# Optimization experiments

Hardware: AMD Instinct MI355X
Metric: run time of the kernel (lower is better)

## Reference

```python
import jax, jax.numpy as jnp
import numpy as np

B = 16       # number of point clouds
N_PER = 2048 # points per cloud
K = 16       # knn neighbors (loop=True -> self included as nearest)
NUM_CLASSES = 10


def _linear_params(key, fan_in, fan_out):
    # torch.nn.Linear default init: U(-1/sqrt(fan_in), 1/sqrt(fan_in))
    kw, kb = jax.random.split(key)
    s = 1.0 / np.sqrt(fan_in)
    W = jax.random.uniform(kw, (fan_in, fan_out), jnp.float32, -s, s)
    b = jax.random.uniform(kb, (fan_out,), jnp.float32, -s, s)
    return W, b


def setup_inputs() -> dict:
    key = jax.random.key(0)
    ks = jax.random.split(key, 7)
    pos = jax.random.normal(ks[0], (B * N_PER, 3), jnp.float32)
    batch = jnp.repeat(jnp.arange(B, dtype=jnp.int64), N_PER)  # sorted graph ids
    W1a, b1a = _linear_params(ks[1], 3 + 3, 32)   # conv1 mlp layer 1 (h=pos -> 3+3)
    W1b, b1b = _linear_params(ks[2], 32, 32)      # conv1 mlp layer 2
    W2a, b2a = _linear_params(ks[3], 32 + 3, 32)  # conv2 mlp layer 1
    W2b, b2b = _linear_params(ks[4], 32, 32)      # conv2 mlp layer 2
    Wc, bc = _linear_params(ks[5], 32, NUM_CLASSES)
    return dict(pos=pos, batch=batch,
                W1a=W1a, b1a=b1a, W1b=W1b, b1b=b1b,
                W2a=W2a, b2a=b2a, W2b=W2b, b2b=b2b,
                Wc=Wc, bc=bc)


def _knn_idx(p):
    # p: [n,3] -> [n,K] indices of K nearest points (self included, dist 0)
    d2 = jnp.sum((p[:, None, :] - p[None, :, :]) ** 2, axis=-1)  # [n,n]
    _, idx = jax.lax.top_k(-d2, K)
    return idx


def _pointnet_layer(h, p, idx, Wa, ba, Wb, bb):
    # single graph: h [n,C], p [n,3], idx [n,K]
    h_j = h[idx]                           # gather neighbor features [n,K,C]
    spatial = p[idx] - p[:, None, :]       # pos_j - pos_i [n,K,3]
    x = jnp.concatenate([h_j, spatial], axis=-1)
    x = jax.nn.relu(x @ Wa + ba) @ Wb + bb # per-edge MLP
    return jnp.max(x, axis=1)              # max aggregation over neighbors


def reference(pos, batch, W1a, b1a, W1b, b1b, W2a, b2a, W2b, b2b, Wc, bc):
    # batch is sorted with equal-sized graphs -> reshape to [B, n, 3]
    p = pos.reshape(B, N_PER, 3)
    idx = jax.vmap(_knn_idx)(p)  # [B, n, K] dynamic knn graph
    layer = jax.vmap(_pointnet_layer, in_axes=(0, 0, 0, None, None, None, None))
    h = jax.nn.relu(layer(p, p, idx, W1a, b1a, W1b, b1b))   # [B, n, 32]
    h = jax.nn.relu(layer(h, p, idx, W2a, b2a, W2b, b2b))   # [B, n, 32]
    g = jnp.max(h, axis=1)                                   # global_max_pool [B, 32]
    return g @ Wc + bc                                       # [B, num_classes]
```

## Files before the change

kernel.cpp:

```cpp
#include <hip/hip_runtime.h>
#include <hip/hip_bf16.h>
#include <cstdint>

#define NCLOUDS 16
#define N_PER   2048
#define KNN_K   16
#define CAP     48

typedef unsigned long long u64;
#define INFF __builtin_inff()

template <int J>
__device__ __forceinline__ int ixor(int x) {
    if constexpr (J == 1)
        return __builtin_amdgcn_update_dpp(0, x, 0xB1, 0xF, 0xF, true);
    else if constexpr (J == 2)
        return __builtin_amdgcn_update_dpp(0, x, 0x4E, 0xF, 0xF, true);
    else if constexpr (J <= 16)
        return __builtin_amdgcn_ds_swizzle(x, (J << 10) | 0x1F);
    else
        return __shfl_xor(x, 32);
}
template <int J> __device__ __forceinline__ float fxor(float x) {
    return __int_as_float(ixor<J>(__float_as_int(x)));
}
template <int J> __device__ __forceinline__ u64 uxor(u64 x) {
    const int lo = ixor<J>((int)(x & 0xffffffffULL));
    const int hi = ixor<J>((int)(x >> 32));
    return ((u64)(unsigned)hi << 32) | (unsigned)lo;
}

__device__ __forceinline__ float dpp_max16(float x) {
    x = fmaxf(x, __int_as_float(__builtin_amdgcn_update_dpp(0, __float_as_int(x), 0xB1, 0xF, 0xF, true)));
    x = fmaxf(x, __int_as_float(__builtin_amdgcn_update_dpp(0, __float_as_int(x), 0x4E, 0xF, 0xF, true)));
    x = fmaxf(x, __int_as_float(__builtin_amdgcn_update_dpp(0, __float_as_int(x), 0x141, 0xF, 0xF, true)));
    x = fmaxf(x, __int_as_float(__builtin_amdgcn_update_dpp(0, __float_as_int(x), 0x140, 0xF, 0xF, true)));
    return x;
}

__global__ __launch_bounds__(512) void knn_kernel(const float* __restrict__ pos,
                                                  int* __restrict__ knn_out,
                                                  const float* __restrict__ W1a,
                                                  const float* __restrict__ b1a,
                                                  float* __restrict__ w1,
                                                  float* __restrict__ v1,
                                                  float* __restrict__ gbuf,
                                                  int* __restrict__ counter)
{
    __shared__ float qshare[3][32];
    __shared__ float smA[4][2][8][16];
    __shared__ u64   buf[4][8][CAP];
    __shared__ int   cnt[4][8];

    const int cloud = blockIdx.x >> 6;
    const int qblk  = blockIdx.x & 63;
    const int tid   = threadIdx.x;
    const int wave  = tid >> 6;
    const int lane  = tid & 63;
    const int H     = wave & 1;
    const int pr    = wave >> 1;

    const int b0 = cloud * N_PER;

    if (blockIdx.x == 0) {
        if (tid < NCLOUDS * 32) gbuf[tid] = 0.0f;
        if (tid == 0) *counter = 0;
    }

    if (tid < 32) {
        const float* qp = pos + (size_t)(b0 + qblk * 32 + tid) * 3;
        qshare[0][tid] = qp[0];
        qshare[1][tid] = qp[1];
        qshare[2][tid] = qp[2];
        ((int*)cnt)[tid] = 0;
    }

    float cx[16], cy[16], cz[16], sc[16];
#pragma unroll
    for (int jj = 0; jj < 16; ++jj) {
        const int c = H * 1024 + jj * 64 + lane;
        const float* p = pos + (size_t)(b0 + c) * 3;
        cx[jj] = p[0]; cy[jj] = p[1]; cz[jj] = p[2];
        sc[jj] = fmaf(cz[jj], cz[jj], fmaf(cy[jj], cy[jj], cx[jj] * cx[jj]));
    }
    __syncthreads();

#pragma unroll 1
    for (int t = 0; t < 4; ++t) {
        const int qg0 = pr * 8 + 2 * t, qg1 = qg0 + 1;
        const float Q0x = qshare[0][qg0], Q0y = qshare[1][qg0], Q0z = qshare[2][qg0];
        const float Q1x = qshare[0][qg1], Q1y = qshare[1][qg1], Q1z = qshare[2][qg1];
        const float A0x = -2.0f * Q0x, A0y = -2.0f * Q0y, A0z = -2.0f * Q0z;
        const float A1x = -2.0f * Q1x, A1y = -2.0f * Q1y, A1z = -2.0f * Q1z;
        float v0 = INFF, v1r = INFF;
#pragma unroll
        for (int jj = 0; jj < 16; ++jj) {
            float e0 = fmaf(cx[jj], A0x, sc[jj]);
            float e1 = fmaf(cx[jj], A1x, sc[jj]);
            e0 = fmaf(cy[jj], A0y, e0);  e1 = fmaf(cy[jj], A1y, e1);
            e0 = fmaf(cz[jj], A0z, e0);  e1 = fmaf(cz[jj], A1z, e1);
            v0 = fminf(v0, e0);          v1r = fminf(v1r, e1);
        }
#define FS(K, J) { const float o0 = fxor<J>(v0), o1 = fxor<J>(v1r);             \
                   const bool km = (((lane & J) == 0) == ((lane & K) == 0));    \
                   v0 = km ? fminf(v0, o0) : fmaxf(v0, o0);                     \
                   v1r = km ? fminf(v1r, o1) : fmaxf(v1r, o1); }
        FS(2,1)
        FS(4,2) FS(4,1)
        FS(8,4) FS(8,2) FS(8,1)
        FS(16,8) FS(16,4) FS(16,2) FS(16,1)
        FS(32,16) FS(32,8) FS(32,4) FS(32,2) FS(32,1)
        FS(64,32) FS(64,16) FS(64,8) FS(64,4) FS(64,2) FS(64,1)
#undef FS
        if (lane < 16) {
            smA[pr][H][2 * t][lane]     = v0;
            smA[pr][H][2 * t + 1][lane] = v1r;
        }
    }
    __syncthreads();

#pragma unroll 1
    for (int t = 0; t < 4; ++t) {
        const int q0 = 2 * t, q1 = q0 + 1;
        float a0 = -INFF, a1 = -INFF, b0v = -INFF, b1v = -INFF;
        if (lane > 0 && lane <= 16) {
            a0 = smA[pr][0][q0][lane - 1];
            a1 = smA[pr][0][q1][lane - 1];
        }
        if (lane < 16) {
            b0v = smA[pr][1][q0][15 - lane];
            b1v = smA[pr][1][q1][15 - lane];
        }
        float m0 = (lane <= 16) ? fmaxf(a0, b0v) : INFF;
        float m1 = (lane <= 16) ? fmaxf(a1, b1v) : INFF;
        m0 = fminf(m0, fxor<1>(m0));   m1 = fminf(m1, fxor<1>(m1));
        m0 = fminf(m0, fxor<2>(m0));   m1 = fminf(m1, fxor<2>(m1));
        m0 = fminf(m0, fxor<4>(m0));   m1 = fminf(m1, fxor<4>(m1));
        m0 = fminf(m0, fxor<8>(m0));   m1 = fminf(m1, fxor<8>(m1));
        m0 = fminf(m0, fxor<16>(m0));  m1 = fminf(m1, fxor<16>(m1));
        m0 = fminf(m0, fxor<32>(m0));  m1 = fminf(m1, fxor<32>(m1));

        const int qg0 = pr * 8 + q0, qg1 = pr * 8 + q1;
        const float Q0x = qshare[0][qg0], Q0y = qshare[1][qg0], Q0z = qshare[2][qg0];
        const float Q1x = qshare[0][qg1], Q1y = qshare[1][qg1], Q1z = qshare[2][qg1];
        const float qq0 = fmaf(Q0z, Q0z, fmaf(Q0y, Q0y, Q0x * Q0x));
        const float qq1 = fmaf(Q1z, Q1z, fmaf(Q1y, Q1y, Q1x * Q1x));
        const float T0 = (m0 + qq0) * (1.0f + 1e-5f) + 1e-4f;
        const float T1 = (m1 + qq1) * (1.0f + 1e-5f) + 1e-4f;

#pragma unroll
        for (int jj = 0; jj < 16; ++jj) {
            const int c = H * 1024 + jj * 64 + lane;
            const float dx0 = __fsub_rn(Q0x, cx[jj]);
            const float dy0 = __fsub_rn(Q0y, cy[jj]);
            const float dz0 = __fsub_rn(Q0z, cz[jj]);
            const float d20 = __fadd_rn(__fadd_rn(__fmul_rn(dx0, dx0), __fmul_rn(dy0, dy0)),
                                        __fmul_rn(dz0, dz0));
            if (d20 <= T0) {
                const int slot = atomicAdd(&cnt[pr][q0], 1);
                if (slot < CAP)
                    buf[pr][q0][slot] = ((u64)__float_as_uint(d20) << 32) | (unsigned)c;
            }
            const float dx1 = __fsub_rn(Q1x, cx[jj]);
            const float dy1 = __fsub_rn(Q1y, cy[jj]);
            const float dz1 = __fsub_rn(Q1z, cz[jj]);
            const float d21 = __fadd_rn(__fadd_rn(__fmul_rn(dx1, dx1), __fmul_rn(dy1, dy1)),
                                        __fmul_rn(dz1, dz1));
            if (d21 <= T1) {
                const int slot = atomicAdd(&cnt[pr][q1], 1);
                if (slot < CAP)
                    buf[pr][q1][slot] = ((u64)__float_as_uint(d21) << 32) | (unsigned)c;
            }
        }
    }
    __syncthreads();

#pragma unroll 1
    for (int s = 0; s < 2; ++s) {
        const int q0 = H * 4 + 2 * s, q1 = q0 + 1;
        const int n0 = min(cnt[pr][q0], CAP);
        const int n1 = min(cnt[pr][q1], CAP);
        u64 k0 = (lane < n0) ? buf[pr][q0][lane] : ~0ULL;
        u64 k1 = (lane < n1) ? buf[pr][q1][lane] : ~0ULL;
#define US(K, J) { const u64 o0 = uxor<J>(k0), o1 = uxor<J>(k1);                \
                   const bool km = (((lane & J) == 0) == ((lane & K) == 0));    \
                   const u64 l0 = k0 < o0 ? k0 : o0, h0 = k0 < o0 ? o0 : k0;    \
                   k0 = km ? l0 : h0;                                           \
                   const u64 l1 = k1 < o1 ? k1 : o1, h1 = k1 < o1 ? o1 : k1;    \
                   k1 = km ? l1 : h1; }
        US(2,1)
        US(4,2) US(4,1)
        US(8,4) US(8,2) US(8,1)
        US(16,8) US(16,4) US(16,2) US(16,1)
        US(32,16) US(32,8) US(32,4) US(32,2) US(32,1)
        US(64,32) US(64,16) US(64,8) US(64,4) US(64,2) US(64,1)
#undef US
        if (lane < KNN_K) {
            knn_out[((size_t)b0 + qblk * 32 + pr * 8 + q0) * KNN_K + lane] =
                b0 + (int)(unsigned)(k0 & 0xffffffffu);
            knn_out[((size_t)b0 + qblk * 32 + pr * 8 + q1) * KNN_K + lane] =
                b0 + (int)(unsigned)(k1 & 0xffffffffu);
        }
    }

    {
        const int pt = tid >> 4;
        const int kk = tid & 15;
        const int gp = b0 + qblk * 32 + pt;
        const float p0 = pos[3 * (size_t)gp + 0];
        const float p1 = pos[3 * (size_t)gp + 1];
        const float p2 = pos[3 * (size_t)gp + 2];
        float vA = 0.f, vB = 0.f;
        float wA = b1a[kk], wB = b1a[16 + kk];
#pragma unroll
        for (int d = 0; d < 3; ++d) {
            const float pd = d == 0 ? p0 : (d == 1 ? p1 : p2);
            wA = fmaf(pd, W1a[d * 32 + kk],        wA);
            wB = fmaf(pd, W1a[d * 32 + 16 + kk],   wB);
            vA = fmaf(pd, W1a[(3 + d) * 32 + kk],      vA);
            vB = fmaf(pd, W1a[(3 + d) * 32 + 16 + kk], vB);
        }
        w1[(size_t)gp * 32 + kk]      = wA + vA;
        w1[(size_t)gp * 32 + 16 + kk] = wB + vB;
        v1[(size_t)gp * 32 + kk]      = vA;
        v1[(size_t)gp * 32 + 16 + kk] = vB;
    }
}

template <int MODE>
__global__ __launch_bounds__(256) void layer_kernel(
    const int*   __restrict__ knn,
    const float* __restrict__ Wb, const float* __restrict__ bb,
    const float* __restrict__ w,  const float* __restrict__ v,
    const float* __restrict__ pos,
    const float* __restrict__ Wna, const float* __restrict__ bna,
    float* __restrict__ outA, float* __restrict__ outB,
    const float* __restrict__ Wc, const float* __restrict__ bc,
    float* __restrict__ gbuf, int* __restrict__ counter,
    float* __restrict__ out)
{
    __shared__ float wst[256 * 36];
    __shared__ float vst[16 * 36];
    __shared__ int   jl[256];
    __shared__ int   lastFlag;

    const int tid = threadIdx.x;
    const int gth = blockIdx.x * 256 + tid;
    const int P0  = blockIdx.x * 16;

    jl[tid] = knn[gth];
    __syncthreads();

#pragma unroll
    for (int s = 0; s < 8; ++s) {
        const int r = s * 32 + (tid >> 3);
        const int i = tid & 7;
        const float4 t4 = *(const float4*)(w + (size_t)jl[r] * 32 + i * 4);
        *(float4*)&wst[r * 36 + i * 4] = t4;
    }
    if (tid < 128) {
        const int r = tid >> 3, i = tid & 7;
        const float4 t4 = *(const float4*)(v + (size_t)(P0 + r) * 32 + i * 4);
        *(float4*)&vst[r * 36 + i * 4] = t4;
    }
    __syncthreads();

    const int k  = tid & 15;
    const int pl = tid >> 4;

    float hid[32];
#pragma unroll
    for (int i = 0; i < 8; ++i) {
        const float4 a = *(const float4*)&wst[tid * 36 + i * 4];
        const float4 b = *(const float4*)&vst[pl  * 36 + i * 4];
        hid[4 * i + 0] = fmaxf(a.x - b.x, 0.0f);
        hid[4 * i + 1] = fmaxf(a.y - b.y, 0.0f);
        hid[4 * i + 2] = fmaxf(a.z - b.z, 0.0f);
        hid[4 * i + 3] = fmaxf(a.w - b.w, 0.0f);
    }

    float o[32];
#pragma unroll
    for (int c2 = 0; c2 < 32; ++c2) o[c2] = bb[c2];
#pragma unroll
    for (int c = 0; c < 32; ++c) {
        const float hc = hid[c];
        const float* row = Wb + c * 32;
#pragma unroll
        for (int c2 = 0; c2 < 32; ++c2) o[c2] = fmaf(hc, row[c2], o[c2]);
    }

    float out0 = 0.0f, out1 = 0.0f;
#pragma unroll
    for (int c2 = 0; c2 < 32; ++c2) {
        const float s = dpp_max16(o[c2]);
        if ((c2 & 15) == k) { if (c2 < 16) out0 = s; else out1 = s; }
    }
    out0 = fmaxf(out0, 0.0f);
    out1 = fmaxf(out1, 0.0f);

    __syncthreads();
    float* hs = wst;
    hs[pl * 32 + k]      = out0;
    hs[pl * 32 + 16 + k] = out1;
    __syncthreads();

    if constexpr (MODE == 1) {
        const int p = gth >> 4;
        float accA = bna[k], accB = bna[16 + k];
#pragma unroll
        for (int c = 0; c < 32; ++c) {
            const float hc = hs[pl * 32 + c];
            accA = fmaf(hc, Wna[c * 32 + k],      accA);
            accB = fmaf(hc, Wna[c * 32 + 16 + k], accB);
        }
        float vA = 0.f, vB = 0.f;
#pragma unroll
        for (int d = 0; d < 3; ++d) {
            const float pd = pos[3 * (size_t)p + d];
            vA = fmaf(pd, Wna[(32 + d) * 32 + k],      vA);
            vB = fmaf(pd, Wna[(32 + d) * 32 + 16 + k], vB);
        }
        outA[(size_t)p * 32 + k]      = accA + vA;
        outA[(size_t)p * 32 + 16 + k] = accB + vB;
        outB[(size_t)p * 32 + k]      = vA;
        outB[(size_t)p * 32 + 16 + k] = vB;
    } else {
        if (tid < 32) {
            float m = hs[tid];
#pragma unroll
            for (int p2 = 1; p2 < 16; ++p2) m = fmaxf(m, hs[p2 * 32 + tid]);
            const int cloud = P0 >> 11;
            atomicMax((int*)&gbuf[cloud * 32 + tid], __float_as_int(m));
        }
        __syncthreads();
        if (tid == 0) {
            __threadfence();
            lastFlag = (atomicAdd(counter, 1) == (int)gridDim.x - 1);
        }
        __syncthreads();
        if (lastFlag) {
            float* gl = wst;
            for (int t = tid; t < NCLOUDS * 32; t += 256)
                gl[t] = __int_as_float(atomicMax((int*)&gbuf[t], 0));
            __syncthreads();
            if (tid < NCLOUDS * 10) {
                const int cl = tid / 10, cls = tid - cl * 10;
                float s2 = bc[cls];
#pragma unroll
                for (int c = 0; c < 32; ++c)
                    s2 = fmaf(gl[cl * 32 + c], Wc[c * 10 + cls], s2);
                out[tid] = s2;
            }
        }
    }
}

extern "C" void kernel_launch(void* const* d_in, const int* in_sizes, int n_in,
                              void* d_out, int out_size, void* d_ws, size_t ws_size,
                              hipStream_t stream)
{
    const float* pos = (const float*)d_in[0];
    const float* W1a = (const float*)d_in[2];
    const float* b1a = (const float*)d_in[3];
    const float* W1b = (const float*)d_in[4];
    const float* b1b = (const float*)d_in[5];
    const float* W2a = (const float*)d_in[6];
    const float* b2a = (const float*)d_in[7];
    const float* W2b = (const float*)d_in[8];
    const float* b2b = (const float*)d_in[9];
    const float* Wc  = (const float*)d_in[10];
    const float* bc  = (const float*)d_in[11];

    int*   knn     = (int*)d_ws;
    float* w1      = (float*)((char*)d_ws + (size_t)(2  << 20));
    float* v1      = (float*)((char*)d_ws + (size_t)(6  << 20));
    float* w2      = (float*)((char*)d_ws + (size_t)(10 << 20));
    float* v2      = (float*)((char*)d_ws + (size_t)(14 << 20));
    float* gbuf    = (float*)((char*)d_ws + (size_t)(18 << 20));
    int*   counter = (int*)((char*)d_ws + (size_t)(18 << 20) + 4096);
    float* out     = (float*)d_out;

    const int npts = NCLOUDS * N_PER;

    knn_kernel<<<dim3(NCLOUDS * 64), dim3(512), 0, stream>>>(
        pos, knn, W1a, b1a, w1, v1, gbuf, counter);
    layer_kernel<1><<<dim3(npts * KNN_K / 256), dim3(256), 0, stream>>>(
        knn, W1b, b1b, w1, v1, pos, W2a, b2a, w2, v2,
        nullptr, nullptr, nullptr, nullptr, nullptr);
    layer_kernel<2><<<dim3(npts * KNN_K / 256), dim3(256), 0, stream>>>(
        knn, W2b, b2b, w2, v2, pos, nullptr, nullptr, nullptr, nullptr,
        Wc, bc, gbuf, counter, out);
}
```

Measured before the change: 138.7 us.

## Fuse both point layers into one cooperative kernel with grid syncs

Replaces the two per-layer kernel launches with a single cooperative kernel of 512 blocks, each handling 64 points. Grid-wide syncs separate layer 1, layer 2 and the final classifier, and the knn indices are kept in registers across both layers. The edge MLP now reads gathered neighbour features straight from global memory instead of staging them in shared memory. This removes one launch and the last-block counter, at the cost of grid-sync overhead and less parallelism (4 sequential edge passes per thread, limited occupancy). The old two-kernel path stays as a fallback if the cooperative launch fails.

New measurement: 383.1 us. +176.2%, slower.

```diff
diff --git a/kernel.cpp b/kernel.cpp
--- a/kernel.cpp
+++ b/kernel.cpp
@@ -1,6 +1,9 @@
 #include <hip/hip_runtime.h>
 #include <hip/hip_bf16.h>
+#include <hip/hip_cooperative_groups.h>
 #include <cstdint>
+
+namespace cg = cooperative_groups;
 
 #define NCLOUDS 16
 #define N_PER   2048
@@ -227,6 +230,142 @@
     }
 }
 
+__device__ __forceinline__ void edge_mlp(const float* __restrict__ w,
+                                         const float* __restrict__ v,
+                                         int j, int p, int k,
+                                         const float* __restrict__ Wb,
+                                         const float* __restrict__ bb,
+                                         float& out0, float& out1)
+{
+    const float4* w4 = (const float4*)w;
+    const float4* v4 = (const float4*)v;
+    float hid[32];
+#pragma unroll
+    for (int i = 0; i < 8; ++i) {
+        const float4 a = w4[(size_t)j * 8 + i];
+        const float4 b = v4[(size_t)p * 8 + i];
+        hid[4 * i + 0] = fmaxf(a.x - b.x, 0.0f);
+        hid[4 * i + 1] = fmaxf(a.y - b.y, 0.0f);
+        hid[4 * i + 2] = fmaxf(a.z - b.z, 0.0f);
+        hid[4 * i + 3] = fmaxf(a.w - b.w, 0.0f);
+    }
+    float o[32];
+#pragma unroll
+    for (int c2 = 0; c2 < 32; ++c2) o[c2] = bb[c2];
+#pragma unroll
+    for (int c = 0; c < 32; ++c) {
+        const float hc = hid[c];
+        const float* row = Wb + c * 32;
+#pragma unroll
+        for (int c2 = 0; c2 < 32; ++c2) o[c2] = fmaf(hc, row[c2], o[c2]);
+    }
+    out0 = 0.0f; out1 = 0.0f;
+#pragma unroll
+    for (int c2 = 0; c2 < 32; ++c2) {
+        const float s = dpp_max16(o[c2]);
+        if ((c2 & 15) == k) { if (c2 < 16) out0 = s; else out1 = s; }
+    }
+    out0 = fmaxf(out0, 0.0f);
+    out1 = fmaxf(out1, 0.0f);
+}
+
+__global__ __launch_bounds__(256, 2) void mega_kernel(
+    const int*   __restrict__ knn,  const float* __restrict__ pos,
+    const float* __restrict__ W1b,  const float* __restrict__ b1b,
+    const float* __restrict__ w1,   const float* __restrict__ v1,
+    const float* __restrict__ W2a,  const float* __restrict__ b2a,
+    float* __restrict__ w2,         float* __restrict__ v2,
+    const float* __restrict__ W2b,  const float* __restrict__ b2b,
+    const float* __restrict__ Wc,   const float* __restrict__ bc,
+    float* __restrict__ gbuf,       float* __restrict__ out)
+{
+    cg::grid_group grid = cg::this_grid();
+    __shared__ float hs[64][32];
+    __shared__ float gl[NCLOUDS * 32];
+
+    const int tid = threadIdx.x;
+    const int P0  = blockIdx.x * 64;
+    const int k   = tid & 15;
+    const int prl = tid >> 4;
+
+    int jreg[4];
+#pragma unroll
+    for (int i = 0; i < 4; ++i)
+        jreg[i] = knn[(size_t)(P0 + i * 16 + prl) * KNN_K + k];
+
+#pragma unroll 1
+    for (int i = 0; i < 4; ++i) {
+        const int pl = i * 16 + prl;
+        float o0, o1;
+        edge_mlp(w1, v1, jreg[i], P0 + pl, k, W1b, b1b, o0, o1);
+        hs[pl][k]      = o0;
+        hs[pl][16 + k] = o1;
+    }
+    __syncthreads();
+
+#pragma unroll 1
+    for (int i = 0; i < 4; ++i) {
+        const int pl = i * 16 + prl;
+        const int p  = P0 + pl;
+        float accA = b2a[k], accB = b2a[16 + k];
+#pragma unroll
+        for (int c = 0; c < 32; ++c) {
+            const float hc = hs[pl][c];
+            accA = fmaf(hc, W2a[c * 32 + k],      accA);
+            accB = fmaf(hc, W2a[c * 32 + 16 + k], accB);
+        }
+        float vA = 0.f, vB = 0.f;
+#pragma unroll
+        for (int d = 0; d < 3; ++d) {
+            const float pd = pos[3 * (size_t)p + d];
+            vA = fmaf(pd, W2a[(32 + d) * 32 + k],      vA);
+            vB = fmaf(pd, W2a[(32 + d) * 32 + 16 + k], vB);
+        }
+        w2[(size_t)p * 32 + k]      = accA + vA;
+        w2[(size_t)p * 32 + 16 + k] = accB + vB;
+        v2[(size_t)p * 32 + k]      = vA;
+        v2[(size_t)p * 32 + 16 + k] = vB;
+    }
+
+    __threadfence();
+    grid.sync();
+
+#pragma unroll 1
+    for (int i = 0; i < 4; ++i) {
+        const int pl = i * 16 + prl;
+        float o0, o1;
+        edge_mlp(w2, v2, jreg[i], P0 + pl, k, W2b, b2b, o0, o1);
+        hs[pl][k]      = o0;
+        hs[pl][16 + k] = o1;
+    }
+    __syncthreads();
+
+    if (tid < 32) {
+        float m = hs[0][tid];
+#pragma unroll
+        for (int r = 1; r < 64; ++r) m = fmaxf(m, hs[r][tid]);
+        const int cloud = blockIdx.x >> 5;
+        atomicMax((int*)&gbuf[cloud * 32 + tid], __float_as_int(m));
+    }
+
+    __threadfence();
+    grid.sync();
+
+    if (blockIdx.x == 0) {
+        for (int t = tid; t < NCLOUDS * 32; t += 256)
+            gl[t] = __int_as_float(atomicMax((int*)&gbuf[t], 0));
+        __syncthreads();
+        if (tid < NCLOUDS * 10) {
+            const int cl = tid / 10, cls = tid - cl * 10;
+            float s2 = bc[cls];
+#pragma unroll
+            for (int c = 0; c < 32; ++c)
+                s2 = fmaf(gl[cl * 32 + c], Wc[c * 10 + cls], s2);
+            out[tid] = s2;
+        }
+    }
+}
+
 template <int MODE>
 __global__ __launch_bounds__(256) void layer_kernel(
     const int*   __restrict__ knn,
@@ -239,78 +378,30 @@
     float* __restrict__ gbuf, int* __restrict__ counter,
     float* __restrict__ out)
 {
-    __shared__ float wst[256 * 36];
-    __shared__ float vst[16 * 36];
-    __shared__ int   jl[256];
+    __shared__ float hsf[16][32];
+    __shared__ float glf[NCLOUDS * 32];
     __shared__ int   lastFlag;
 
     const int tid = threadIdx.x;
     const int gth = blockIdx.x * 256 + tid;
     const int P0  = blockIdx.x * 16;
-
-    jl[tid] = knn[gth];
-    __syncthreads();
-
-#pragma unroll
-    for (int s = 0; s < 8; ++s) {
-        const int r = s * 32 + (tid >> 3);
-        const int i = tid & 7;
-        const float4 t4 = *(const float4*)(w + (size_t)jl[r] * 32 + i * 4);
-        *(float4*)&wst[r * 36 + i * 4] = t4;
-    }
-    if (tid < 128) {
-        const int r = tid >> 3, i = tid & 7;
-        const float4 t4 = *(const float4*)(v + (size_t)(P0 + r) * 32 + i * 4);
-        *(float4*)&vst[r * 36 + i * 4] = t4;
-    }
-    __syncthreads();
-
-    const int k  = tid & 15;
+    const int p   = gth >> 4;
+    const int k   = gth & 15;
+    const int j   = knn[gth];
+
+    float o0, o1;
+    edge_mlp(w, v, j, p, k, Wb, bb, o0, o1);
+
     const int pl = tid >> 4;
-
-    float hid[32];
-#pragma unroll
-    for (int i = 0; i < 8; ++i) {
-        const float4 a = *(const float4*)&wst[tid * 36 + i * 4];
-        const float4 b = *(const float4*)&vst[pl  * 36 + i * 4];
-        hid[4 * i + 0] = fmaxf(a.x - b.x, 0.0f);
-        hid[4 * i + 1] = fmaxf(a.y - b.y, 0.0f);
-        hid[4 * i + 2] = fmaxf(a.z - b.z, 0.0f);
-        hid[4 * i + 3] = fmaxf(a.w - b.w, 0.0f);
-    }
-
-    float o[32];
-#pragma unroll
-    for (int c2 = 0; c2 < 32; ++c2) o[c2] = bb[c2];
-#pragma unroll
-    for (int c = 0; c < 32; ++c) {
-        const float hc = hid[c];
-        const float* row = Wb + c * 32;
-#pragma unroll
-        for (int c2 = 0; c2 < 32; ++c2) o[c2] = fmaf(hc, row[c2], o[c2]);
-    }
-
-    float out0 = 0.0f, out1 = 0.0f;
-#pragma unroll
-    for (int c2 = 0; c2 < 32; ++c2) {
-        const float s = dpp_max16(o[c2]);
-        if ((c2 & 15) == k) { if (c2 < 16) out0 = s; else out1 = s; }
-    }
-    out0 = fmaxf(out0, 0.0f);
-    out1 = fmaxf(out1, 0.0f);
-
-    __syncthreads();
-    float* hs = wst;
-    hs[pl * 32 + k]      = out0;
-    hs[pl * 32 + 16 + k] = out1;
+    hsf[pl][k]      = o0;
+    hsf[pl][16 + k] = o1;
     __syncthreads();
 
     if constexpr (MODE == 1) {
-        const int p = gth >> 4;
         float accA = bna[k], accB = bna[16 + k];
 #pragma unroll
         for (int c = 0; c < 32; ++c) {
-            const float hc = hs[pl * 32 + c];
+            const float hc = hsf[pl][c];
             accA = fmaf(hc, Wna[c * 32 + k],      accA);
             accB = fmaf(hc, Wna[c * 32 + 16 + k], accB);
         }
@@ -327,9 +418,9 @@
         outB[(size_t)p * 32 + 16 + k] = vB;
     } else {
         if (tid < 32) {
-            float m = hs[tid];
-#pragma unroll
-            for (int p2 = 1; p2 < 16; ++p2) m = fmaxf(m, hs[p2 * 32 + tid]);
+            float m = hsf[0][tid];
+#pragma unroll
+            for (int p2 = 1; p2 < 16; ++p2) m = fmaxf(m, hsf[p2][tid]);
             const int cloud = P0 >> 11;
             atomicMax((int*)&gbuf[cloud * 32 + tid], __float_as_int(m));
         }
@@ -340,16 +431,15 @@
         }
         __syncthreads();
         if (lastFlag) {
-            float* gl = wst;
             for (int t = tid; t < NCLOUDS * 32; t += 256)
-                gl[t] = __int_as_float(atomicMax((int*)&gbuf[t], 0));
+                glf[t] = __int_as_float(atomicMax((int*)&gbuf[t], 0));
             __syncthreads();
             if (tid < NCLOUDS * 10) {
                 const int cl = tid / 10, cls = tid - cl * 10;
                 float s2 = bc[cls];
 #pragma unroll
                 for (int c = 0; c < 32; ++c)
-                    s2 = fmaf(gl[cl * 32 + c], Wc[c * 10 + cls], s2);
+                    s2 = fmaf(glf[cl * 32 + c], Wc[c * 10 + cls], s2);
                 out[tid] = s2;
             }
         }
@@ -385,10 +475,19 @@
 
     knn_kernel<<<dim3(NCLOUDS * 64), dim3(512), 0, stream>>>(
         pos, knn, W1a, b1a, w1, v1, gbuf, counter);
-    layer_kernel<1><<<dim3(npts * KNN_K / 256), dim3(256), 0, stream>>>(
-        knn, W1b, b1b, w1, v1, pos, W2a, b2a, w2, v2,
-        nullptr, nullptr, nullptr, nullptr, nullptr);
-    layer_kernel<2><<<dim3(npts * KNN_K / 256), dim3(256), 0, stream>>>(
-        knn, W2b, b2b, w2, v2, pos, nullptr, nullptr, nullptr, nullptr,
-        Wc, bc, gbuf, counter, out);
-}
+
+    void* args[] = { &knn, &pos, &W1b, &b1b, &w1, &v1, &W2a, &b2a,
+                     &w2, &v2, &W2b, &b2b, &Wc, &bc, &gbuf, &out };
+    hipError_t cerr = hipLaunchCooperativeKernel((const void*)mega_kernel,
+                                                 dim3(512), dim3(256), args,
+                                                 0, stream);
+    if (cerr != hipSuccess) {
+        (void)hipGetLastError();
+        layer_kernel<1><<<dim3(npts * KNN_K / 256), dim3(256), 0, stream>>>(
+            knn, W1b, b1b, w1, v1, pos, W2a, b2a, w2, v2,
+            nullptr, nullptr, nullptr, nullptr, nullptr);
+        layer_kernel<2><<<dim3(npts * KNN_K / 256), dim3(256), 0, stream>>>(
+            knn, W2b, b2b, w2, v2, pos, nullptr, nullptr, nullptr, nullptr,
+            Wc, bc, gbuf, counter, out);
+    }
+}
```
